# Kernel tuning notes

Hardware: AMD Instinct MI355X
Metric: run time of the kernel (lower is better)

The kernel has to match this reference:

```python
import jax, jax.numpy as jnp
import numpy as np

N = 100000   # nodes
E = 1600000  # edges
G = 2048     # graphs in batch
NC = 204     # n_classes
DEPTH = 5
EPS = 1e-5


def setup_inputs() -> dict:
    key = jax.random.key(0)
    ks = jax.random.split(key, 20)
    rn = lambda k, s, sc=0.05: (jax.random.normal(k, s, jnp.float32) * sc)
    inp = {
        "h": jax.random.normal(ks[0], (N, 78), jnp.float32),
        "edge_src": jax.random.randint(ks[1], (E,), 0, N),
        "edge_dst": jax.random.randint(ks[2], (E,), 0, N),
        "graph_ids": jnp.sort(jax.random.randint(ks[3], (N,), 0, G)),
        "W1": rn(ks[4], (78, 128)),
        "b1": rn(ks[5], (128,)),
        "g1_gamma": jnp.ones((128,), jnp.float32),
        "g1_beta": jnp.zeros((128,), jnp.float32),
        "Wg": rn(ks[6], (DEPTH - 1, 128, 128)),
        "bg": rn(ks[7], (DEPTH - 1, 128)),
        "g_gamma": jnp.ones((DEPTH - 1, 128), jnp.float32),
        "g_beta": jnp.zeros((DEPTH - 1, 128), jnp.float32),
        "fc1_W": rn(ks[8], (128, 512)),
        "fc1_b": rn(ks[9], (512,)),
        "bn1_gamma": jnp.ones((512,), jnp.float32),
        "bn1_beta": jnp.zeros((512,), jnp.float32),
        "lin_W": rn(ks[10], (512, 256)),
        "lin_b": rn(ks[11], (256,)),
        "lbn_gamma": jnp.ones((256,), jnp.float32),
        "lbn_beta": jnp.zeros((256,), jnp.float32),
        "fc2_W": rn(ks[12], (256, 408)),
        "fc2_b": rn(ks[13], (408,)),
    }
    return inp


def _bn(x, gamma, beta):
    # torch BatchNorm1d training-mode normalization: biased batch var, eps=1e-5
    mu = jnp.mean(x, axis=0)
    var = jnp.var(x, axis=0)
    return (x - mu) * jax.lax.rsqrt(var + EPS) * gamma + beta


def _gin(h, src, dst, W, b):
    # DGL GINConv (eps=0, sum agg): apply_func(h + sum_neigh(h)); module adds apply_func(h)
    agg = jax.ops.segment_sum(h[src], dst, num_segments=h.shape[0])  # [N, d]
    return (h + agg) @ W + b + (h @ W + b)


def reference(h, edge_src, edge_dst, graph_ids, W1, b1, g1_gamma, g1_beta,
              Wg, bg, g_gamma, g_beta, fc1_W, fc1_b, bn1_gamma, bn1_beta,
              lin_W, lin_b, lbn_gamma, lbn_beta, fc2_W, fc2_b):
    x = jax.nn.relu(_bn(_gin(h, edge_src, edge_dst, W1, b1), g1_gamma, g1_beta))
    for i in range(DEPTH - 1):
        x = jax.nn.relu(_bn(_gin(x, edge_src, edge_dst, Wg[i], bg[i]),
                            g_gamma[i], g_beta[i]))
    # sum readout over nodes of each graph -> [G, 128]
    xg = jax.ops.segment_sum(x, graph_ids, num_segments=G)
    x = jax.nn.relu(_bn(xg @ fc1_W + fc1_b, bn1_gamma, bn1_beta))
    x = jax.nn.relu(_bn(x @ lin_W + lin_b, lbn_gamma, lbn_beta))
    logits = x @ fc2_W + fc2_b          # [G, 2*NC]
    return jax.nn.sigmoid(logits[:, -NC:])  # [G, NC]
```

## Files before the change

kernel.cpp:

```cpp
#include <hip/hip_runtime.h>
#include <hip/hip_bf16.h>
#include <math.h>

#define N_NODES 100000
#define N_EDGES 1600000
#define N_GRAPHS 2048
#define NCLS 204
#define EPS_BN 1e-5f
#define NBUCK ((N_NODES + 255) / 256)
#define BIN_CHUNK 8192

typedef __attribute__((ext_vector_type(8))) short short8;
typedef __attribute__((ext_vector_type(4))) float f32x4;

__device__ __forceinline__ float bf_lo(uint v) { union { uint i; float f; } c; c.i = v << 16; return c.f; }
__device__ __forceinline__ float bf_hi(uint v) { union { uint i; float f; } c; c.i = v & 0xffff0000u; return c.f; }
__device__ __forceinline__ ushort f2bf(float v) {
  __hip_bfloat16 b = __float2bfloat16(v);
  return *reinterpret_cast<ushort*>(&b);
}
__device__ __forceinline__ uint pack2(float a, float b) {
  return (uint)f2bf(a) | ((uint)f2bf(b) << 16);
}

__global__ void k_degree(const int* __restrict__ dst, int* __restrict__ deg, int E) {
  int i = blockIdx.x * blockDim.x + threadIdx.x;
  if (i < E) atomicAdd(&deg[dst[i]], 1);
}

__global__ __launch_bounds__(256) void k_scan_part(const int* __restrict__ deg,
                                                   int* __restrict__ part, int n) {
  __shared__ int red[256];
  int t = threadIdx.x;
  int base = blockIdx.x * 1024 + t * 4;
  int s = 0;
  if (base + 4 <= n) {
    int4 v = *reinterpret_cast<const int4*>(deg + base);
    s = v.x + v.y + v.z + v.w;
  } else {
    for (int k = 0; k < 4; k++) if (base + k < n) s += deg[base + k];
  }
  red[t] = s;
  __syncthreads();
  for (int d = 128; d > 0; d >>= 1) {
    if (t < d) red[t] += red[t + d];
    __syncthreads();
  }
  if (t == 0) part[blockIdx.x] = red[0];
}

__global__ __launch_bounds__(128) void k_scan_off(int* __restrict__ part, int nb) {
  __shared__ int sh[128];
  int t = threadIdx.x;
  sh[t] = (t < nb) ? part[t] : 0;
  __syncthreads();
  for (int d = 1; d < 128; d <<= 1) {
    int v = (t >= d) ? sh[t - d] : 0;
    __syncthreads();
    sh[t] += v;
    __syncthreads();
  }
  if (t < nb) part[t] = (t == 0) ? 0 : sh[t - 1];
}

__global__ __launch_bounds__(256) void k_scan_write(const int* __restrict__ deg,
                                                    const int* __restrict__ part,
                                                    int* __restrict__ row_ptr, int n) {
  __shared__ int red[256];
  int t = threadIdx.x;
  int base = blockIdx.x * 1024 + t * 4;
  int v[4];
  int s = 0;
  for (int k = 0; k < 4; k++) {
    v[k] = (base + k < n) ? deg[base + k] : 0;
    s += v[k];
  }
  red[t] = s;
  __syncthreads();
  for (int d = 1; d < 256; d <<= 1) {
    int x = (t >= d) ? red[t - d] : 0;
    __syncthreads();
    red[t] += x;
    __syncthreads();
  }
  int run = part[blockIdx.x] + ((t == 0) ? 0 : red[t - 1]);
  for (int k = 0; k < 4; k++) {
    if (base + k < n) row_ptr[base + k] = run;
    run += v[k];
  }
  if (blockIdx.x == gridDim.x - 1 && t == 255) row_ptr[n] = run;
}

__global__ void k_init_cursor(const int* __restrict__ row_ptr, int* __restrict__ cursor) {
  int b = blockIdx.x * blockDim.x + threadIdx.x;
  if (b < NBUCK) cursor[b] = row_ptr[b * 256];
}

__global__ __launch_bounds__(256) void k_bin(const int* __restrict__ src,
                                             const int* __restrict__ dst,
                                             int* __restrict__ cursor,
                                             uint2* __restrict__ staging, int E) {
  __shared__ int hist[NBUCK];
  __shared__ int base_s[NBUCK];
  int t = threadIdx.x;
  int e0 = blockIdx.x * BIN_CHUNK;
  for (int b = t; b < NBUCK; b += 256) hist[b] = 0;
  __syncthreads();
  for (int e = e0 + t; e < min(e0 + BIN_CHUNK, E); e += 256)
    atomicAdd(&hist[dst[e] >> 8], 1);
  __syncthreads();
  for (int b = t; b < NBUCK; b += 256) {
    int hh = hist[b];
    if (hh > 0) base_s[b] = atomicAdd(&cursor[b], hh);
    hist[b] = 0;
  }
  __syncthreads();
  for (int e = e0 + t; e < min(e0 + BIN_CHUNK, E); e += 256) {
    int d = dst[e];
    int b = d >> 8;
    int r = atomicAdd(&hist[b], 1);
    staging[base_s[b] + r] = make_uint2((uint)src[e], (uint)d);
  }
}

__global__ __launch_bounds__(256) void k_place(const uint2* __restrict__ staging,
                                               const int* __restrict__ row_ptr,
                                               int* __restrict__ csr, int nNodes) {
  __shared__ int cur[256];
  int t = threadIdx.x;
  int n0 = blockIdx.x * 256;
  int nend = min(n0 + 256, nNodes);
  if (n0 + t < nend) cur[t] = row_ptr[n0 + t];
  __syncthreads();
  int s = row_ptr[n0];
  int e = row_ptr[nend];
  for (int i = s + t; i < e; i += 256) {
    uint2 ed = staging[i];
    int pos = atomicAdd(&cur[ed.y - n0], 1);
    csr[pos] = (int)ed.x;
  }
}

__global__ void k_conv_h(const float* __restrict__ h, uint* __restrict__ hb, int nNodes) {
  int i = blockIdx.x * blockDim.x + threadIdx.x;
  if (i < nNodes * 64) {
    int n = i >> 6, cp = i & 63;
    int c = cp * 2;
    float a = (c < 78) ? h[(size_t)n * 78 + c] : 0.0f;
    float b = (c + 1 < 78) ? h[(size_t)n * 78 + c + 1] : 0.0f;
    hb[i] = pack2(a, b);
  }
}

__global__ void k_prep_wt(const float* __restrict__ W, ushort* __restrict__ Wt, int K) {
  int i = blockIdx.x * blockDim.x + threadIdx.x;
  if (i < 128 * 128) {
    int n = i >> 7, k = i & 127;
    float v = (k < K) ? W[(size_t)k * 128 + n] : 0.0f;
    Wt[i] = f2bf(v);
  }
}

__global__ void k_prep_wt_gen(const float* __restrict__ W, int wld, int col_off, int nkeep,
                              int K, ushort* __restrict__ Wt, int total) {
  int i = blockIdx.x * blockDim.x + threadIdx.x;
  if (i < total) {
    int n = i / K, k = i - n * K;
    float v = (n < nkeep) ? W[(size_t)k * wld + col_off + n] : 0.0f;
    Wt[i] = f2bf(v);
  }
}

template <bool NRM>
__global__ __launch_bounds__(256) void k_agg_f(const uint* __restrict__ y,
                                               const int* __restrict__ row_ptr,
                                               const int* __restrict__ csr,
                                               const float* __restrict__ Ac,
                                               const float* __restrict__ Bc,
                                               uint* __restrict__ M, int nNodes) {
  int n = blockIdx.x * 4 + (threadIdx.x >> 6);
  if (n >= nNodes) return;
  int l = threadIdx.x & 63;
  float A0 = 1.f, B0 = 0.f, A1 = 1.f, B1 = 0.f;
  if (NRM) { A0 = Ac[2 * l]; B0 = Bc[2 * l]; A1 = Ac[2 * l + 1]; B1 = Bc[2 * l + 1]; }

  auto flo = [&](uint v) { float x = bf_lo(v); return NRM ? fmaxf(x * A0 + B0, 0.f) : x; };
  auto fhi = [&](uint v) { float x = bf_hi(v); return NRM ? fmaxf(x * A1 + B1, 0.f) : x; };

  uint self = y[(size_t)n * 64 + l];
  float a0 = 2.0f * flo(self);
  float a1 = 2.0f * fhi(self);
  int s = row_ptr[n], e = row_ptr[n + 1];

  for (int base = s; base < e; base += 64) {
    int cnt = e - base;
    if (cnt > 64) cnt = 64;
    int myidx = (base + l < e) ? csr[base + l] : 0;
    int j = 0;
    for (; j + 4 <= cnt; j += 4) {
      int i0 = __shfl(myidx, j);
      int i1 = __shfl(myidx, j + 1);
      int i2 = __shfl(myidx, j + 2);
      int i3 = __shfl(myidx, j + 3);
      uint v0 = y[(size_t)i0 * 64 + l];
      uint v1 = y[(size_t)i1 * 64 + l];
      uint v2 = y[(size_t)i2 * 64 + l];
      uint v3 = y[(size_t)i3 * 64 + l];
      a0 += flo(v0) + flo(v1) + flo(v2) + flo(v3);
      a1 += fhi(v0) + fhi(v1) + fhi(v2) + fhi(v3);
    }
    for (; j < cnt; j++) {
      int i0 = __shfl(myidx, j);
      uint v = y[(size_t)i0 * 64 + l];
      a0 += flo(v);
      a1 += fhi(v);
    }
  }
  M[(size_t)n * 64 + l] = pack2(a0, a1);
}

#define SWZ(row, boff) ((boff) ^ (((row) & 7) << 4))
__global__ __launch_bounds__(256) void k_gemm_mfma(const ushort* __restrict__ A,
                                                   const ushort* __restrict__ Wt,
                                                   const float* __restrict__ bias, float bscale,
                                                   ushort* __restrict__ Y, int Mrows,
                                                   float* __restrict__ gsum,
                                                   float* __restrict__ gsq) {
  __shared__ ushort As[128 * 128];
  __shared__ ushort Bs[128 * 128];
  __shared__ float sred[4][128], qred[4][128];
  int t = threadIdx.x;
  int r0 = blockIdx.x * 128;
  char* Ab = (char*)As;
  char* Bb = (char*)Bs;

  for (int it = 0; it < 8; it++) {
    int e = it * 256 + t;
    int row = e >> 4, seg = e & 15;
    uint4 va = make_uint4(0, 0, 0, 0);
    int gr = r0 + row;
    if (gr < Mrows) va = *reinterpret_cast<const uint4*>(A + (size_t)gr * 128 + seg * 8);
    *reinterpret_cast<uint4*>(Ab + row * 256 + SWZ(row, seg * 16)) = va;
    uint4 vb = *reinterpret_cast<const uint4*>(Wt + (size_t)row * 128 + seg * 8);
    *reinterpret_cast<uint4*>(Bb + row * 256 + SWZ(row, seg * 16)) = vb;
  }
  __syncthreads();

  int wi = t >> 6;
  int l = t & 63;
  int lr = l & 15;
  int kp = l >> 4;

  f32x4 acc[2][8];
#pragma unroll
  for (int mi = 0; mi < 2; mi++)
#pragma unroll
    for (int ni = 0; ni < 8; ni++) acc[mi][ni] = (f32x4){0.f, 0.f, 0.f, 0.f};

#pragma unroll
  for (int ki = 0; ki < 4; ki++) {
    short8 a[2], b[8];
#pragma unroll
    for (int mi = 0; mi < 2; mi++) {
      int row = wi * 32 + mi * 16 + lr;
      a[mi] = *reinterpret_cast<const short8*>(Ab + row * 256 + SWZ(row, ki * 64 + kp * 16));
    }
#pragma unroll
    for (int ni = 0; ni < 8; ni++) {
      int row = ni * 16 + lr;
      b[ni] = *reinterpret_cast<const short8*>(Bb + row * 256 + SWZ(row, ki * 64 + kp * 16));
    }
#pragma unroll
    for (int mi = 0; mi < 2; mi++)
#pragma unroll
      for (int ni = 0; ni < 8; ni++)
        acc[mi][ni] = __builtin_amdgcn_mfma_f32_16x16x32_bf16(a[mi], b[ni], acc[mi][ni], 0, 0, 0);
  }

  float s_part[8], q_part[8];
#pragma unroll
  for (int ni = 0; ni < 8; ni++) { s_part[ni] = 0.f; q_part[ni] = 0.f; }

#pragma unroll
  for (int mi = 0; mi < 2; mi++) {
    int rbase = r0 + wi * 32 + mi * 16 + kp * 4;
#pragma unroll
    for (int ni = 0; ni < 8; ni++) {
      int col = ni * 16 + lr;
      float bb = bscale * bias[col];
#pragma unroll
      for (int j = 0; j < 4; j++) {
        int r = rbase + j;
        if (r < Mrows) {
          float yv = acc[mi][ni][j] + bb;
          Y[(size_t)r * 128 + col] = f2bf(yv);
          s_part[ni] += yv;
          q_part[ni] += yv * yv;
        }
      }
    }
  }

#pragma unroll
  for (int ni = 0; ni < 8; ni++) {
    s_part[ni] += __shfl_xor(s_part[ni], 16, 64);
    s_part[ni] += __shfl_xor(s_part[ni], 32, 64);
    q_part[ni] += __shfl_xor(q_part[ni], 16, 64);
    q_part[ni] += __shfl_xor(q_part[ni], 32, 64);
  }
  if (kp == 0) {
#pragma unroll
    for (int ni = 0; ni < 8; ni++) {
      sred[wi][ni * 16 + lr] = s_part[ni];
      qred[wi][ni * 16 + lr] = q_part[ni];
    }
  }
  __syncthreads();
  if (t < 128) {
    float S = sred[0][t] + sred[1][t] + sred[2][t] + sred[3][t];
    float Q = qred[0][t] + qred[1][t] + qred[2][t] + qred[3][t];
    atomicAdd(&gsum[t], S);
    atomicAdd(&gsq[t], Q);
  }
}

template <int AMODE, int OMODE>
__global__ __launch_bounds__(256) void k_head_mfma(const void* __restrict__ Aptr,
                                                   int Mrows, int K,
                                                   const ushort* __restrict__ Wt,
                                                   const float* __restrict__ bias,
                                                   int col_off, int ncols,
                                                   const float* __restrict__ nAc,
                                                   const float* __restrict__ nBc,
                                                   void* __restrict__ Yout, int Nld,
                                                   float* __restrict__ gsum,
                                                   float* __restrict__ gsq) {
  __shared__ ushort As[128 * 128];
  __shared__ ushort Bs[128 * 128];
  __shared__ float sred[4][128], qred[4][128];
  int t = threadIdx.x;
  int r0 = blockIdx.y * 128;
  int c0 = blockIdx.x * 128;
  char* Ab = (char*)As;
  char* Bb = (char*)Bs;

  int wi = t >> 6;
  int l = t & 63;
  int lr = l & 15;
  int kp = l >> 4;

  f32x4 acc[2][8];
#pragma unroll
  for (int mi = 0; mi < 2; mi++)
#pragma unroll
    for (int ni = 0; ni < 8; ni++) acc[mi][ni] = (f32x4){0.f, 0.f, 0.f, 0.f};

  for (int k0 = 0; k0 < K; k0 += 128) {
    if (k0) __syncthreads();
    for (int it = 0; it < 8; it++) {
      int e = it * 256 + t;
      int row = e >> 4, seg = e & 15;
      int gr = r0 + row;
      uint4 va;
      if (AMODE == 0) {
        const float* Af = (const float*)Aptr;
        float4 f0 = {0.f, 0.f, 0.f, 0.f}, f1 = {0.f, 0.f, 0.f, 0.f};
        if (gr < Mrows) {
          f0 = *reinterpret_cast<const float4*>(Af + (size_t)gr * K + k0 + seg * 8);
          f1 = *reinterpret_cast<const float4*>(Af + (size_t)gr * K + k0 + seg * 8 + 4);
        }
        va.x = pack2(f0.x, f0.y); va.y = pack2(f0.z, f0.w);
        va.z = pack2(f1.x, f1.y); va.w = pack2(f1.z, f1.w);
      } else {
        const uint* Au = (const uint*)Aptr;
        uint4 r4 = make_uint4(0, 0, 0, 0);
        if (gr < Mrows) r4 = *reinterpret_cast<const uint4*>(Au + (size_t)gr * (K >> 1) + ((k0 + seg * 8) >> 1));
        int c = k0 + seg * 8;
        uint uu[4] = {r4.x, r4.y, r4.z, r4.w};
#pragma unroll
        for (int q = 0; q < 4; q++) {
          float aa = fmaxf(bf_lo(uu[q]) * nAc[c + 2 * q] + nBc[c + 2 * q], 0.f);
          float bb = fmaxf(bf_hi(uu[q]) * nAc[c + 2 * q + 1] + nBc[c + 2 * q + 1], 0.f);
          uu[q] = pack2(aa, bb);
        }
        va = make_uint4(uu[0], uu[1], uu[2], uu[3]);
      }
      *reinterpret_cast<uint4*>(Ab + row * 256 + SWZ(row, seg * 16)) = va;
      uint4 vb = *reinterpret_cast<const uint4*>(Wt + (size_t)(c0 + row) * K + k0 + seg * 8);
      *reinterpret_cast<uint4*>(Bb + row * 256 + SWZ(row, seg * 16)) = vb;
    }
    __syncthreads();

#pragma unroll
    for (int ki = 0; ki < 4; ki++) {
      short8 a[2], b[8];
#pragma unroll
      for (int mi = 0; mi < 2; mi++) {
        int row = wi * 32 + mi * 16 + lr;
        a[mi] = *reinterpret_cast<const short8*>(Ab + row * 256 + SWZ(row, ki * 64 + kp * 16));
      }
#pragma unroll
      for (int ni = 0; ni < 8; ni++) {
        int row = ni * 16 + lr;
        b[ni] = *reinterpret_cast<const short8*>(Bb + row * 256 + SWZ(row, ki * 64 + kp * 16));
      }
#pragma unroll
      for (int mi = 0; mi < 2; mi++)
#pragma unroll
        for (int ni = 0; ni < 8; ni++)
          acc[mi][ni] = __builtin_amdgcn_mfma_f32_16x16x32_bf16(a[mi], b[ni], acc[mi][ni], 0, 0, 0);
    }
  }

  if (OMODE == 0) {
    float s_part[8], q_part[8];
#pragma unroll
    for (int ni = 0; ni < 8; ni++) { s_part[ni] = 0.f; q_part[ni] = 0.f; }
#pragma unroll
    for (int mi = 0; mi < 2; mi++) {
      int rbase = r0 + wi * 32 + mi * 16 + kp * 4;
#pragma unroll
      for (int ni = 0; ni < 8; ni++) {
        int gc = c0 + ni * 16 + lr;
        float bb = bias[col_off + gc];
#pragma unroll
        for (int j = 0; j < 4; j++) {
          int r = rbase + j;
          if (r < Mrows) {
            float yv = acc[mi][ni][j] + bb;
            ((ushort*)Yout)[(size_t)r * Nld + gc] = f2bf(yv);
            s_part[ni] += yv;
            q_part[ni] += yv * yv;
          }
        }
      }
    }
#pragma unroll
    for (int ni = 0; ni < 8; ni++) {
      s_part[ni] += __shfl_xor(s_part[ni], 16, 64);
      s_part[ni] += __shfl_xor(s_part[ni], 32, 64);
      q_part[ni] += __shfl_xor(q_part[ni], 16, 64);
      q_part[ni] += __shfl_xor(q_part[ni], 32, 64);
    }
    if (kp == 0) {
#pragma unroll
      for (int ni = 0; ni < 8; ni++) {
        sred[wi][ni * 16 + lr] = s_part[ni];
        qred[wi][ni * 16 + lr] = q_part[ni];
      }
    }
    __syncthreads();
    if (t < 128) {
      float S = sred[0][t] + sred[1][t] + sred[2][t] + sred[3][t];
      float Q = qred[0][t] + qred[1][t] + qred[2][t] + qred[3][t];
      atomicAdd(&gsum[c0 + t], S);
      atomicAdd(&gsq[c0 + t], Q);
    }
  } else {
#pragma unroll
    for (int mi = 0; mi < 2; mi++) {
      int rbase = r0 + wi * 32 + mi * 16 + kp * 4;
#pragma unroll
      for (int ni = 0; ni < 8; ni++) {
        int gc = c0 + ni * 16 + lr;
        if (gc < ncols) {
          float bb = bias[col_off + gc];
#pragma unroll
          for (int j = 0; j < 4; j++) {
            int r = rbase + j;
            if (r < Mrows) {
              float v = acc[mi][ni][j] + bb;
              ((float*)Yout)[(size_t)r * Nld + gc] = 1.0f / (1.0f + expf(-v));
            }
          }
        }
      }
    }
  }
}

__global__ void k_bnparams(const float* __restrict__ sum, const float* __restrict__ sumsq,
                           const float* __restrict__ gamma, const float* __restrict__ beta,
                           float* __restrict__ Ac, float* __restrict__ Bc,
                           int C, float invM) {
  int c = blockIdx.x * blockDim.x + threadIdx.x;
  if (c < C) {
    float mu = sum[c] * invM;
    float var = sumsq[c] * invM - mu * mu;
    float rs = rsqrtf(var + EPS_BN);
    float a = gamma[c] * rs;
    Ac[c] = a;
    Bc[c] = beta[c] - mu * a;
  }
}

__global__ __launch_bounds__(64) void k_readout(const uint* __restrict__ y,
                                                const int* __restrict__ gid,
                                                const float* __restrict__ Ac,
                                                const float* __restrict__ Bc,
                                                float* __restrict__ xg, int nNodes) {
  int l = threadIdx.x;
  int n0 = blockIdx.x * 64;
  int n1 = min(n0 + 64, nNodes);
  if (n0 >= nNodes) return;
  float A0 = Ac[2 * l], B0 = Bc[2 * l], A1 = Ac[2 * l + 1], B1 = Bc[2 * l + 1];
  float a0 = 0, a1 = 0;
  int cur = gid[n0];
  for (int n = n0; n < n1; n++) {
    int g = gid[n];
    if (g != cur) {
      atomicAdd(&xg[(size_t)cur * 128 + 2 * l], a0);
      atomicAdd(&xg[(size_t)cur * 128 + 2 * l + 1], a1);
      a0 = 0; a1 = 0; cur = g;
    }
    uint v = y[(size_t)n * 64 + l];
    a0 += fmaxf(bf_lo(v) * A0 + B0, 0.f);
    a1 += fmaxf(bf_hi(v) * A1 + B1, 0.f);
  }
  atomicAdd(&xg[(size_t)cur * 128 + 2 * l], a0);
  atomicAdd(&xg[(size_t)cur * 128 + 2 * l + 1], a1);
}

extern "C" void kernel_launch(void* const* d_in, const int* in_sizes, int n_in,
                              void* d_out, int out_size, void* d_ws, size_t ws_size,
                              hipStream_t stream) {
  const float* h    = (const float*)d_in[0];
  const int*   esrc = (const int*)d_in[1];
  const int*   edst = (const int*)d_in[2];
  const int*   gid  = (const int*)d_in[3];
  const float* W1   = (const float*)d_in[4];
  const float* b1   = (const float*)d_in[5];
  const float* g1g  = (const float*)d_in[6];
  const float* g1b  = (const float*)d_in[7];
  const float* Wg   = (const float*)d_in[8];
  const float* bg   = (const float*)d_in[9];
  const float* gg   = (const float*)d_in[10];
  const float* gb   = (const float*)d_in[11];
  const float* fc1W = (const float*)d_in[12];
  const float* fc1b = (const float*)d_in[13];
  const float* bn1g = (const float*)d_in[14];
  const float* bn1b = (const float*)d_in[15];
  const float* linW = (const float*)d_in[16];
  const float* linb = (const float*)d_in[17];
  const float* lbng = (const float*)d_in[18];
  const float* lbnb = (const float*)d_in[19];
  const float* fc2W = (const float*)d_in[20];
  const float* fc2b = (const float*)d_in[21];
  float* out = (float*)d_out;

  char* p = (char*)d_ws;
  auto alloc = [&](size_t bytes) {
    char* q = p;
    p += (bytes + 255) & ~(size_t)255;
    return q;
  };
  int* row_ptr = (int*)alloc((N_NODES + 1) * sizeof(int));
  int* cursor  = (int*)alloc(N_NODES * sizeof(int));
  int* part    = (int*)alloc(128 * sizeof(int));
  int* bcur    = (int*)alloc(NBUCK * sizeof(int));
  int* csr     = (int*)alloc(N_EDGES * sizeof(int));
  uint* hb     = (uint*)alloc((size_t)N_NODES * 64 * sizeof(uint));
  uint* Mb     = (uint*)alloc((size_t)N_NODES * 64 * sizeof(uint));
  uint* yb     = (uint*)alloc((size_t)N_NODES * 64 * sizeof(uint));
  ushort* Wt   = (ushort*)alloc(5 * 128 * 128 * sizeof(ushort));
  ushort* fc1Wt = (ushort*)alloc(512 * 128 * sizeof(ushort));
  ushort* linWt = (ushort*)alloc(256 * 512 * sizeof(ushort));
  ushort* fc2Wt = (ushort*)alloc(256 * 256 * sizeof(ushort));
  float* ssum  = (float*)alloc(512 * sizeof(float));
  float* ssq   = (float*)alloc(512 * sizeof(float));
  float* Ac    = (float*)alloc(512 * sizeof(float));
  float* Bc    = (float*)alloc(512 * sizeof(float));
  float* xg    = (float*)alloc((size_t)N_GRAPHS * 128 * sizeof(float));
  uint* y1b    = (uint*)alloc((size_t)N_GRAPHS * 256 * sizeof(uint));
  uint* y2b    = (uint*)alloc((size_t)N_GRAPHS * 128 * sizeof(uint));
  uint2* staging = (uint2*)Mb;

  k_conv_h<<<(N_NODES * 64 + 255) / 256, 256, 0, stream>>>(h, hb, N_NODES);
  k_prep_wt<<<64, 256, 0, stream>>>(W1, Wt, 78);
  for (int l = 0; l < 4; l++)
    k_prep_wt<<<64, 256, 0, stream>>>(Wg + (size_t)l * 128 * 128, Wt + (size_t)(l + 1) * 128 * 128, 128);
  k_prep_wt_gen<<<(512 * 128 + 255) / 256, 256, 0, stream>>>(fc1W, 512, 0, 512, 128, fc1Wt, 512 * 128);
  k_prep_wt_gen<<<(256 * 512 + 255) / 256, 256, 0, stream>>>(linW, 256, 0, 256, 512, linWt, 256 * 512);
  k_prep_wt_gen<<<(256 * 256 + 255) / 256, 256, 0, stream>>>(fc2W, 408, 204, 204, 256, fc2Wt, 256 * 256);

  const int NB = (N_NODES + 1023) / 1024;
  hipMemsetAsync(cursor, 0, N_NODES * sizeof(int), stream);
  k_degree<<<(N_EDGES + 255) / 256, 256, 0, stream>>>(edst, cursor, N_EDGES);
  k_scan_part<<<NB, 256, 0, stream>>>(cursor, part, N_NODES);
  k_scan_off<<<1, 128, 0, stream>>>(part, NB);
  k_scan_write<<<NB, 256, 0, stream>>>(cursor, part, row_ptr, N_NODES);
  k_init_cursor<<<(NBUCK + 255) / 256, 256, 0, stream>>>(row_ptr, bcur);
  k_bin<<<(N_EDGES + BIN_CHUNK - 1) / BIN_CHUNK, 256, 0, stream>>>(esrc, edst, bcur,
                                                                   staging, N_EDGES);
  k_place<<<NBUCK, 256, 0, stream>>>(staging, row_ptr, csr, N_NODES);

  const float invN = 1.0f / (float)N_NODES;
  const float invG = 1.0f / (float)N_GRAPHS;

  for (int layer = 0; layer < 5; layer++) {
    const ushort* Wl = Wt + (size_t)layer * 128 * 128;
    const float* bl  = (layer == 0) ? b1 : bg + (size_t)(layer - 1) * 128;
    const float* gl  = (layer == 0) ? g1g : gg + (size_t)(layer - 1) * 128;
    const float* bl2 = (layer == 0) ? g1b : gb + (size_t)(layer - 1) * 128;

    if (layer == 0)
      k_agg_f<false><<<(N_NODES + 3) / 4, 256, 0, stream>>>(hb, row_ptr, csr, nullptr, nullptr,
                                                            Mb, N_NODES);
    else
      k_agg_f<true><<<(N_NODES + 3) / 4, 256, 0, stream>>>(yb, row_ptr, csr, Ac, Bc,
                                                           Mb, N_NODES);
    hipMemsetAsync(ssum, 0, 128 * sizeof(float), stream);
    hipMemsetAsync(ssq, 0, 128 * sizeof(float), stream);
    k_gemm_mfma<<<(N_NODES + 127) / 128, 256, 0, stream>>>((const ushort*)Mb, Wl, bl, 2.0f,
                                                           (ushort*)yb, N_NODES, ssum, ssq);
    k_bnparams<<<1, 128, 0, stream>>>(ssum, ssq, gl, bl2, Ac, Bc, 128, invN);
  }

  hipMemsetAsync(xg, 0, (size_t)N_GRAPHS * 128 * sizeof(float), stream);
  k_readout<<<(N_NODES + 63) / 64, 64, 0, stream>>>(yb, gid, Ac, Bc, xg, N_NODES);

  hipMemsetAsync(ssum, 0, 512 * sizeof(float), stream);
  hipMemsetAsync(ssq, 0, 512 * sizeof(float), stream);
  k_head_mfma<0, 0><<<dim3(4, 16), 256, 0, stream>>>(xg, N_GRAPHS, 128, fc1Wt, fc1b, 0, 512,
                                                     nullptr, nullptr, y1b, 512, ssum, ssq);
  k_bnparams<<<1, 512, 0, stream>>>(ssum, ssq, bn1g, bn1b, Ac, Bc, 512, invG);

  hipMemsetAsync(ssum, 0, 256 * sizeof(float), stream);
  hipMemsetAsync(ssq, 0, 256 * sizeof(float), stream);
  k_head_mfma<1, 0><<<dim3(2, 16), 256, 0, stream>>>(y1b, N_GRAPHS, 512, linWt, linb, 0, 256,
                                                     Ac, Bc, y2b, 256, ssum, ssq);
  k_bnparams<<<1, 256, 0, stream>>>(ssum, ssq, lbng, lbnb, Ac, Bc, 256, invG);

  k_head_mfma<1, 1><<<dim3(2, 16), 256, 0, stream>>>(y2b, N_GRAPHS, 256, fc2Wt, fc2b, 204, NCLS,
                                                     Ac, Bc, out, NCLS, nullptr, nullptr);
}
```

Before: 763.0 us.

## Slice node features into 16-channel planes and simplify CSR build via bucket counts

```diff
diff --git a/kernel.cpp b/kernel.cpp
--- a/kernel.cpp
+++ b/kernel.cpp
@@ -9,6 +9,8 @@
 #define EPS_BN 1e-5f
 #define NBUCK ((N_NODES + 255) / 256)
 #define BIN_CHUNK 8192
+#define N8 ((size_t)N_NODES * 8)
+#define N16 ((size_t)N_NODES * 16)
 
 typedef __attribute__((ext_vector_type(8))) short short8;
 typedef __attribute__((ext_vector_type(4))) float f32x4;
@@ -23,77 +25,40 @@
   return (uint)f2bf(a) | ((uint)f2bf(b) << 16);
 }
 
-__global__ void k_degree(const int* __restrict__ dst, int* __restrict__ deg, int E) {
-  int i = blockIdx.x * blockDim.x + threadIdx.x;
-  if (i < E) atomicAdd(&deg[dst[i]], 1);
-}
-
-__global__ __launch_bounds__(256) void k_scan_part(const int* __restrict__ deg,
-                                                   int* __restrict__ part, int n) {
-  __shared__ int red[256];
+__global__ __launch_bounds__(256) void k_bin_count(const int* __restrict__ dst,
+                                                   int* __restrict__ bcnt, int E) {
+  __shared__ int hist[NBUCK];
   int t = threadIdx.x;
-  int base = blockIdx.x * 1024 + t * 4;
-  int s = 0;
-  if (base + 4 <= n) {
-    int4 v = *reinterpret_cast<const int4*>(deg + base);
-    s = v.x + v.y + v.z + v.w;
-  } else {
-    for (int k = 0; k < 4; k++) if (base + k < n) s += deg[base + k];
-  }
-  red[t] = s;
-  __syncthreads();
-  for (int d = 128; d > 0; d >>= 1) {
-    if (t < d) red[t] += red[t + d];
+  int e0 = blockIdx.x * BIN_CHUNK;
+  for (int b = t; b < NBUCK; b += 256) hist[b] = 0;
+  __syncthreads();
+  for (int e = e0 + t; e < min(e0 + BIN_CHUNK, E); e += 256)
+    atomicAdd(&hist[dst[e] >> 8], 1);
+  __syncthreads();
+  for (int b = t; b < NBUCK; b += 256)
+    if (hist[b] > 0) atomicAdd(&bcnt[b], hist[b]);
+}
+
+__global__ __launch_bounds__(512) void k_bucket_scan(const int* __restrict__ bcnt,
+                                                     int* __restrict__ bbase,
+                                                     int* __restrict__ bcur) {
+  __shared__ int sh[512];
+  int t = threadIdx.x;
+  int v = (t < NBUCK) ? bcnt[t] : 0;
+  sh[t] = v;
+  __syncthreads();
+  for (int d = 1; d < 512; d <<= 1) {
+    int x = (t >= d) ? sh[t - d] : 0;
     __syncthreads();
-  }
-  if (t == 0) part[blockIdx.x] = red[0];
-}
-
-__global__ __launch_bounds__(128) void k_scan_off(int* __restrict__ part, int nb) {
-  __shared__ int sh[128];
-  int t = threadIdx.x;
-  sh[t] = (t < nb) ? part[t] : 0;
-  __syncthreads();
-  for (int d = 1; d < 128; d <<= 1) {
-    int v = (t >= d) ? sh[t - d] : 0;
+    sh[t] += x;
     __syncthreads();
-    sh[t] += v;
-    __syncthreads();
-  }
-  if (t < nb) part[t] = (t == 0) ? 0 : sh[t - 1];
-}
-
-__global__ __launch_bounds__(256) void k_scan_write(const int* __restrict__ deg,
-                                                    const int* __restrict__ part,
-                                                    int* __restrict__ row_ptr, int n) {
-  __shared__ int red[256];
-  int t = threadIdx.x;
-  int base = blockIdx.x * 1024 + t * 4;
-  int v[4];
-  int s = 0;
-  for (int k = 0; k < 4; k++) {
-    v[k] = (base + k < n) ? deg[base + k] : 0;
-    s += v[k];
-  }
-  red[t] = s;
-  __syncthreads();
-  for (int d = 1; d < 256; d <<= 1) {
-    int x = (t >= d) ? red[t - d] : 0;
-    __syncthreads();
-    red[t] += x;
-    __syncthreads();
-  }
-  int run = part[blockIdx.x] + ((t == 0) ? 0 : red[t - 1]);
-  for (int k = 0; k < 4; k++) {
-    if (base + k < n) row_ptr[base + k] = run;
-    run += v[k];
-  }
-  if (blockIdx.x == gridDim.x - 1 && t == 255) row_ptr[n] = run;
-}
-
-__global__ void k_init_cursor(const int* __restrict__ row_ptr, int* __restrict__ cursor) {
-  int b = blockIdx.x * blockDim.x + threadIdx.x;
-  if (b < NBUCK) cursor[b] = row_ptr[b * 256];
+  }
+  if (t < NBUCK) {
+    bbase[t + 1] = sh[t];
+    int excl = sh[t] - v;
+    bcur[t] = excl;
+    if (t == 0) bbase[0] = 0;
+  }
 }
 
 __global__ __launch_bounds__(256) void k_bin(const int* __restrict__ src,
@@ -123,32 +88,51 @@
   }
 }
 
-__global__ __launch_bounds__(256) void k_place(const uint2* __restrict__ staging,
-                                               const int* __restrict__ row_ptr,
-                                               int* __restrict__ csr, int nNodes) {
+__global__ __launch_bounds__(256) void k_place2(const uint2* __restrict__ staging,
+                                                const int* __restrict__ bbase,
+                                                int* __restrict__ row_ptr,
+                                                int* __restrict__ csr, int nNodes, int E) {
+  __shared__ int cnt[256];
+  __shared__ int scn[256];
   __shared__ int cur[256];
   int t = threadIdx.x;
-  int n0 = blockIdx.x * 256;
-  int nend = min(n0 + 256, nNodes);
-  if (n0 + t < nend) cur[t] = row_ptr[n0 + t];
-  __syncthreads();
-  int s = row_ptr[n0];
-  int e = row_ptr[nend];
+  int b = blockIdx.x;
+  int n0 = b * 256;
+  cnt[t] = 0;
+  __syncthreads();
+  int s = bbase[b], e = bbase[b + 1];
+  for (int i = s + t; i < e; i += 256) atomicAdd(&cnt[staging[i].y - n0], 1);
+  __syncthreads();
+  int v = cnt[t];
+  scn[t] = v;
+  __syncthreads();
+  for (int d = 1; d < 256; d <<= 1) {
+    int x = (t >= d) ? scn[t - d] : 0;
+    __syncthreads();
+    scn[t] += x;
+    __syncthreads();
+  }
+  int excl = scn[t] - v;
+  if (n0 + t < nNodes) row_ptr[n0 + t] = s + excl;
+  cur[t] = s + excl;
+  __syncthreads();
   for (int i = s + t; i < e; i += 256) {
     uint2 ed = staging[i];
     int pos = atomicAdd(&cur[ed.y - n0], 1);
     csr[pos] = (int)ed.x;
   }
+  if (b == 0 && t == 0) row_ptr[nNodes] = E;
 }
 
 __global__ void k_conv_h(const float* __restrict__ h, uint* __restrict__ hb, int nNodes) {
-  int i = blockIdx.x * blockDim.x + threadIdx.x;
-  if (i < nNodes * 64) {
-    int n = i >> 6, cp = i & 63;
-    int c = cp * 2;
+  int j = blockIdx.x * blockDim.x + threadIdx.x;
+  int slice = blockIdx.y;
+  if (j < nNodes * 8) {
+    int n = j >> 3, w = j & 7;
+    int c = slice * 16 + 2 * w;
     float a = (c < 78) ? h[(size_t)n * 78 + c] : 0.0f;
     float b = (c + 1 < 78) ? h[(size_t)n * 78 + c + 1] : 0.0f;
-    hb[i] = pack2(a, b);
+    hb[(size_t)slice * N8 + j] = pack2(a, b);
   }
 }
 
@@ -172,55 +156,53 @@
 }
 
 template <bool NRM>
-__global__ __launch_bounds__(256) void k_agg_f(const uint* __restrict__ y,
+__global__ __launch_bounds__(256) void k_agg_s(const uint* __restrict__ y,
                                                const int* __restrict__ row_ptr,
                                                const int* __restrict__ csr,
                                                const float* __restrict__ Ac,
                                                const float* __restrict__ Bc,
                                                uint* __restrict__ M, int nNodes) {
-  int n = blockIdx.x * 4 + (threadIdx.x >> 6);
+  int slice = blockIdx.x & 7;
+  int nb = blockIdx.x >> 3;
+  int wv = threadIdx.x >> 6;
+  int l = threadIdx.x & 63;
+  int n = nb * 4 + wv;
   if (n >= nNodes) return;
-  int l = threadIdx.x & 63;
+  int cp = l & 7;
+  int slot = l >> 3;
+  const uint* ys = y + (size_t)slice * N8;
+  uint* Ms = M + (size_t)slice * N8;
   float A0 = 1.f, B0 = 0.f, A1 = 1.f, B1 = 0.f;
-  if (NRM) { A0 = Ac[2 * l]; B0 = Bc[2 * l]; A1 = Ac[2 * l + 1]; B1 = Bc[2 * l + 1]; }
-
+  if (NRM) {
+    int c = slice * 16 + 2 * cp;
+    A0 = Ac[c]; B0 = Bc[c]; A1 = Ac[c + 1]; B1 = Bc[c + 1];
+  }
   auto flo = [&](uint v) { float x = bf_lo(v); return NRM ? fmaxf(x * A0 + B0, 0.f) : x; };
   auto fhi = [&](uint v) { float x = bf_hi(v); return NRM ? fmaxf(x * A1 + B1, 0.f) : x; };
 
-  uint self = y[(size_t)n * 64 + l];
-  float a0 = 2.0f * flo(self);
-  float a1 = 2.0f * fhi(self);
   int s = row_ptr[n], e = row_ptr[n + 1];
-
-  for (int base = s; base < e; base += 64) {
-    int cnt = e - base;
-    if (cnt > 64) cnt = 64;
-    int myidx = (base + l < e) ? csr[base + l] : 0;
-    int j = 0;
-    for (; j + 4 <= cnt; j += 4) {
-      int i0 = __shfl(myidx, j);
-      int i1 = __shfl(myidx, j + 1);
-      int i2 = __shfl(myidx, j + 2);
-      int i3 = __shfl(myidx, j + 3);
-      uint v0 = y[(size_t)i0 * 64 + l];
-      uint v1 = y[(size_t)i1 * 64 + l];
-      uint v2 = y[(size_t)i2 * 64 + l];
-      uint v3 = y[(size_t)i3 * 64 + l];
-      a0 += flo(v0) + flo(v1) + flo(v2) + flo(v3);
-      a1 += fhi(v0) + fhi(v1) + fhi(v2) + fhi(v3);
-    }
-    for (; j < cnt; j++) {
-      int i0 = __shfl(myidx, j);
-      uint v = y[(size_t)i0 * 64 + l];
+  float a0 = 0.f, a1 = 0.f;
+  if (slot == 0) {
+    uint v = ys[(size_t)n * 8 + cp];
+    a0 = 2.0f * flo(v);
+    a1 = 2.0f * fhi(v);
+  }
+  for (int base = s; base < e; base += 8) {
+    if (base + slot < e) {
+      int idx = csr[base + slot];
+      uint v = ys[(size_t)idx * 8 + cp];
       a0 += flo(v);
       a1 += fhi(v);
     }
   }
-  M[(size_t)n * 64 + l] = pack2(a0, a1);
+  a0 += __shfl_xor(a0, 8); a1 += __shfl_xor(a1, 8);
+  a0 += __shfl_xor(a0, 16); a1 += __shfl_xor(a1, 16);
+  a0 += __shfl_xor(a0, 32); a1 += __shfl_xor(a1, 32);
+  if (slot == 0) Ms[(size_t)n * 8 + cp] = pack2(a0, a1);
 }
 
 #define SWZ(row, boff) ((boff) ^ (((row) & 7) << 4))
-__global__ __launch_bounds__(256) void k_gemm_mfma(const ushort* __restrict__ A,
+__global__ __launch_bounds__(256) void k_gemm_mfma(const uint* __restrict__ A,
                                                    const ushort* __restrict__ Wt,
                                                    const float* __restrict__ bias, float bscale,
                                                    ushort* __restrict__ Y, int Mrows,
@@ -239,7 +221,8 @@
     int row = e >> 4, seg = e & 15;
     uint4 va = make_uint4(0, 0, 0, 0);
     int gr = r0 + row;
-    if (gr < Mrows) va = *reinterpret_cast<const uint4*>(A + (size_t)gr * 128 + seg * 8);
+    if (gr < Mrows)
+      va = *reinterpret_cast<const uint4*>(A + (size_t)(seg >> 1) * N8 + (size_t)gr * 8 + (seg & 1) * 4);
     *reinterpret_cast<uint4*>(Ab + row * 256 + SWZ(row, seg * 16)) = va;
     uint4 vb = *reinterpret_cast<const uint4*>(Wt + (size_t)row * 128 + seg * 8);
     *reinterpret_cast<uint4*>(Bb + row * 256 + SWZ(row, seg * 16)) = vb;
@@ -288,12 +271,13 @@
     for (int ni = 0; ni < 8; ni++) {
       int col = ni * 16 + lr;
       float bb = bscale * bias[col];
+      ushort* Ys = Y + (size_t)(col >> 4) * N16;
 #pragma unroll
       for (int j = 0; j < 4; j++) {
         int r = rbase + j;
         if (r < Mrows) {
           float yv = acc[mi][ni][j] + bb;
-          Y[(size_t)r * 128 + col] = f2bf(yv);
+          Ys[(size_t)r * 16 + (col & 15)] = f2bf(yv);
           s_part[ni] += yv;
           q_part[ni] += yv * yv;
         }
@@ -503,6 +487,8 @@
   int n0 = blockIdx.x * 64;
   int n1 = min(n0 + 64, nNodes);
   if (n0 >= nNodes) return;
+  const uint* ys = y + (size_t)(l >> 3) * N8;
+  int w = l & 7;
   float A0 = Ac[2 * l], B0 = Bc[2 * l], A1 = Ac[2 * l + 1], B1 = Bc[2 * l + 1];
   float a0 = 0, a1 = 0;
   int cur = gid[n0];
@@ -513,7 +499,7 @@
       atomicAdd(&xg[(size_t)cur * 128 + 2 * l + 1], a1);
       a0 = 0; a1 = 0; cur = g;
     }
-    uint v = y[(size_t)n * 64 + l];
+    uint v = ys[(size_t)n * 8 + w];
     a0 += fmaxf(bf_lo(v) * A0 + B0, 0.f);
     a1 += fmaxf(bf_hi(v) * A1 + B1, 0.f);
   }
@@ -555,13 +541,13 @@
     return q;
   };
   int* row_ptr = (int*)alloc((N_NODES + 1) * sizeof(int));
-  int* cursor  = (int*)alloc(N_NODES * sizeof(int));
-  int* part    = (int*)alloc(128 * sizeof(int));
+  int* bcnt    = (int*)alloc(NBUCK * sizeof(int));
+  int* bbase   = (int*)alloc((NBUCK + 1) * sizeof(int));
   int* bcur    = (int*)alloc(NBUCK * sizeof(int));
   int* csr     = (int*)alloc(N_EDGES * sizeof(int));
-  uint* hb     = (uint*)alloc((size_t)N_NODES * 64 * sizeof(uint));
-  uint* Mb     = (uint*)alloc((size_t)N_NODES * 64 * sizeof(uint));
-  uint* yb     = (uint*)alloc((size_t)N_NODES * 64 * sizeof(uint));
+  uint* hb     = (uint*)alloc(8 * N8 * sizeof(uint));
+  uint* Mb     = (uint*)alloc(8 * N8 * sizeof(uint));
+  uint* yb     = (uint*)alloc(8 * N8 * sizeof(uint));
   ushort* Wt   = (ushort*)alloc(5 * 128 * 128 * sizeof(ushort));
   ushort* fc1Wt = (ushort*)alloc(512 * 128 * sizeof(ushort));
   ushort* linWt = (ushort*)alloc(256 * 512 * sizeof(ushort));
@@ -575,7 +561,10 @@
   uint* y2b    = (uint*)alloc((size_t)N_GRAPHS * 128 * sizeof(uint));
   uint2* staging = (uint2*)Mb;
 
-  k_conv_h<<<(N_NODES * 64 + 255) / 256, 256, 0, stream>>>(h, hb, N_NODES);
+  {
+    dim3 g((N_NODES * 8 + 255) / 256, 8);
+    k_conv_h<<<g, 256, 0, stream>>>(h, hb, N_NODES);
+  }
   k_prep_wt<<<64, 256, 0, stream>>>(W1, Wt, 78);
   for (int l = 0; l < 4; l++)
     k_prep_wt<<<64, 256, 0, stream>>>(Wg + (size_t)l * 128 * 128, Wt + (size_t)(l + 1) * 128 * 128, 128);
@@ -583,20 +572,17 @@
   k_prep_wt_gen<<<(256 * 512 + 255) / 256, 256, 0, stream>>>(linW, 256, 0, 256, 512, linWt, 256 * 512);
   k_prep_wt_gen<<<(256 * 256 + 255) / 256, 256, 0, stream>>>(fc2W, 408, 204, 204, 256, fc2Wt, 256 * 256);
 
-  const int NB = (N_NODES + 1023) / 1024;
-  hipMemsetAsync(cursor, 0, N_NODES * sizeof(int), stream);
-  k_degree<<<(N_EDGES + 255) / 256, 256, 0, stream>>>(edst, cursor, N_EDGES);
-  k_scan_part<<<NB, 256, 0, stream>>>(cursor, part, N_NODES);
-  k_scan_off<<<1, 128, 0, stream>>>(part, NB);
-  k_scan_write<<<NB, 256, 0, stream>>>(cursor, part, row_ptr, N_NODES);
-  k_init_cursor<<<(NBUCK + 255) / 256, 256, 0, stream>>>(row_ptr, bcur);
+  hipMemsetAsync(bcnt, 0, NBUCK * sizeof(int), stream);
+  k_bin_count<<<(N_EDGES + BIN_CHUNK - 1) / BIN_CHUNK, 256, 0, stream>>>(edst, bcnt, N_EDGES);
+  k_bucket_scan<<<1, 512, 0, stream>>>(bcnt, bbase, bcur);
   k_bin<<<(N_EDGES + BIN_CHUNK - 1) / BIN_CHUNK, 256, 0, stream>>>(esrc, edst, bcur,
                                                                    staging, N_EDGES);
-  k_place<<<NBUCK, 256, 0, stream>>>(staging, row_ptr, csr, N_NODES);
+  k_place2<<<NBUCK, 256, 0, stream>>>(staging, bbase, row_ptr, csr, N_NODES, N_EDGES);
 
   const float invN = 1.0f / (float)N_NODES;
   const float invG = 1.0f / (float)N_GRAPHS;
 
+  const int aggGrid = ((N_NODES + 3) / 4) * 8;
   for (int layer = 0; layer < 5; layer++) {
     const ushort* Wl = Wt + (size_t)layer * 128 * 128;
     const float* bl  = (layer == 0) ? b1 : bg + (size_t)(layer - 1) * 128;
@@ -604,14 +590,13 @@
     const float* bl2 = (layer == 0) ? g1b : gb + (size_t)(layer - 1) * 128;
 
     if (layer == 0)
-      k_agg_f<false><<<(N_NODES + 3) / 4, 256, 0, stream>>>(hb, row_ptr, csr, nullptr, nullptr,
-                                                            Mb, N_NODES);
+      k_agg_s<false><<<aggGrid, 256, 0, stream>>>(hb, row_ptr, csr, nullptr, nullptr,
+                                                  Mb, N_NODES);
     else
-      k_agg_f<true><<<(N_NODES + 3) / 4, 256, 0, stream>>>(yb, row_ptr, csr, Ac, Bc,
-                                                           Mb, N_NODES);
+      k_agg_s<true><<<aggGrid, 256, 0, stream>>>(yb, row_ptr, csr, Ac, Bc, Mb, N_NODES);
     hipMemsetAsync(ssum, 0, 128 * sizeof(float), stream);
     hipMemsetAsync(ssq, 0, 128 * sizeof(float), stream);
-    k_gemm_mfma<<<(N_NODES + 127) / 128, 256, 0, stream>>>((const ushort*)Mb, Wl, bl, 2.0f,
+    k_gemm_mfma<<<(N_NODES + 127) / 128, 256, 0, stream>>>(Mb, Wl, bl, 2.0f,
                                                            (ushort*)yb, N_NODES, ssum, ssq);
     k_bnparams<<<1, 128, 0, stream>>>(ssum, ssq, gl, bl2, Ac, Bc, 128, invN);
   }
```

After: 1.537 ms. +101.4%, slower.
